# Performance work log

Measured on AMD Instinct MI355X. Metric: run time of the kernel, lower is better.

## Reference

```python
import jax, jax.numpy as jnp
import numpy as np


def setup_inputs() -> dict:
    key = jax.random.key(0)
    ks = jax.random.split(key, 7)
    B = 32768
    x = jax.random.normal(ks[0], (B, 1, 28, 28), dtype=jnp.float32)
    # learned params (AtomicLinear weight/bias per layer)
    w1 = jax.random.normal(ks[1], (128, 784), dtype=jnp.float32)
    b1 = jax.random.normal(ks[2], (128,), dtype=jnp.float32)
    w2 = jax.random.normal(ks[3], (256, 128), dtype=jnp.float32)
    b2 = jax.random.normal(ks[4], (256,), dtype=jnp.float32)
    w3 = jax.random.normal(ks[5], (10, 256), dtype=jnp.float32)
    b3 = jax.random.normal(ks[6], (10,), dtype=jnp.float32)
    return {"x": x, "w1": w1, "b1": b1, "w2": w2, "b2": b2, "w3": w3, "b3": b3}


def reference(x, w1, b1, w2, b2, w3, b3):
    # AtomicLinear: (x[:,None,:] * W) gathered by a random permutation over
    # in_features, then summed over that axis. Summation is permutation-
    # invariant, so this is exactly x @ W.T + b.
    B = x.shape[0]
    h = x.reshape(B, -1)                      # [B, 784]
    h = jax.nn.relu(h @ w1.T + b1)            # [B, 128]
    h = jax.nn.relu(h @ w2.T + b2)            # [B, 256]
    logits = h @ w3.T + b3                    # [B, 10]
    return jax.nn.log_softmax(logits, axis=1)
```

## Files before the change

### kernel.cpp

```cpp
#include <hip/hip_runtime.h>
#include <math.h>


#define TPB 512
#define BROWS 64

typedef __attribute__((ext_vector_type(8))) short bf16x8;
typedef __attribute__((ext_vector_type(4))) short bf16x4;
typedef __attribute__((ext_vector_type(4))) float f32x4;

static __device__ inline short f2bf(float f) {
    union { float f; unsigned u; } v; v.f = f;
    unsigned r = v.u + 0x7fffu + ((v.u >> 16) & 1u);
    return (short)(r >> 16);
}
static __device__ inline bf16x4 cvt4(float4 a) {
    bf16x4 r; r[0]=f2bf(a.x); r[1]=f2bf(a.y); r[2]=f2bf(a.z); r[3]=f2bf(a.w); return r;
}
static __device__ inline bf16x8 cvt8(float4 a, float4 b) {
    bf16x8 r;
    r[0]=f2bf(a.x); r[1]=f2bf(a.y); r[2]=f2bf(a.z); r[3]=f2bf(a.w);
    r[4]=f2bf(b.x); r[5]=f2bf(b.y); r[6]=f2bf(b.z); r[7]=f2bf(b.w);
    return r;
}
static __device__ inline float4 ld4g(const float* p, bool ok) {
    return ok ? *reinterpret_cast<const float4*>(p) : make_float4(0.f, 0.f, 0.f, 0.f);
}

__global__ __launch_bounds__(TPB, 4) void mnist_mfma_v2(
    const float* __restrict__ x,
    const float* __restrict__ w1,
    const float* __restrict__ b1,
    const float* __restrict__ w2,
    const float* __restrict__ b2,
    const float* __restrict__ w3,
    const float* __restrict__ b3,
    float* __restrict__ out)
{
    __shared__ __align__(16) char smem[40 * 1024];
    short* const s_w  = (short*)(smem);
    short* const s_x  = (short*)(smem + 16 * 1024);
    short* const s_h1 = (short*)(smem + 20 * 1024);
    short* const s_h2 = (short*)(smem);
    short* const s_w3 = (short*)(smem + 32 * 1024);

    const int t    = threadIdx.x;
    const int lane = t & 63;
    const int wv   = t >> 6;
    const int mi   = wv & 3;
    const int nh   = wv >> 2;
    const int l15  = lane & 15;
    const int l4   = lane >> 4;
    const int row0 = blockIdx.x * BROWS;

    const int xr = t >> 3, xs = t & 7;
    const int wn = t >> 2, ws = t & 3;

    f32x4 acc1[4];
    #pragma unroll
    for (int f = 0; f < 4; ++f) acc1[f] = (f32x4){0.f, 0.f, 0.f, 0.f};

    float4 xa = ld4g(&x[(size_t)(row0 + xr) * 784 + xs * 4], true);
    float4 wa = ld4g(&w1[(size_t)wn * 784 + ws * 8], true);
    float4 wb = ld4g(&w1[(size_t)wn * 784 + ws * 8 + 4], true);

    for (int kt = 0; kt < 25; ++kt) {
        __syncthreads();
        *reinterpret_cast<bf16x4*>(&s_x[xr * 32 + xs * 4]) = cvt4(xa);
        *reinterpret_cast<bf16x8*>(&s_w[wn * 32 + ws * 8]) = cvt8(wa, wb);
        if (kt < 24) {
            const int k0 = (kt + 1) * 32;
            xa = ld4g(&x[(size_t)(row0 + xr) * 784 + k0 + xs * 4], k0 + xs * 4 < 784);
            const bool okw = k0 + ws * 8 < 784;
            wa = ld4g(&w1[(size_t)wn * 784 + k0 + ws * 8], okw);
            wb = ld4g(&w1[(size_t)wn * 784 + k0 + ws * 8 + 4], okw);
        }
        __syncthreads();
        const bf16x8 a = *reinterpret_cast<const bf16x8*>(&s_x[(16 * mi + l15) * 32 + l4 * 8]);
        #pragma unroll
        for (int f = 0; f < 4; ++f) {
            const bf16x8 b = *reinterpret_cast<const bf16x8*>(
                &s_w[(nh * 64 + f * 16 + l15) * 32 + l4 * 8]);
            acc1[f] = __builtin_amdgcn_mfma_f32_16x16x32_bf16(a, b, acc1[f], 0, 0, 0);
        }
    }

    #pragma unroll
    for (int f = 0; f < 4; ++f) {
        const int c  = nh * 64 + f * 16 + l15;
        const float bc = b1[c];
        #pragma unroll
        for (int i = 0; i < 4; ++i) {
            const int r = 16 * mi + l4 * 4 + i;
            float h = acc1[f][i] + bc;
            h = h > 0.f ? h : 0.f;
            s_h1[r * 128 + ((((c >> 3) ^ (r & 7)) << 3) | (c & 7))] = f2bf(h);
        }
    }

    f32x4 acc2[8];
    #pragma unroll
    for (int f = 0; f < 8; ++f) acc2[f] = (f32x4){0.f, 0.f, 0.f, 0.f};

    float4 w2a0 = ld4g(&w2[(size_t)(t >> 2) * 128 + (t & 3) * 8], true);
    float4 w2b0 = ld4g(&w2[(size_t)(t >> 2) * 128 + (t & 3) * 8 + 4], true);
    float4 w2a1 = ld4g(&w2[(size_t)(128 + (t >> 2)) * 128 + (t & 3) * 8], true);
    float4 w2b1 = ld4g(&w2[(size_t)(128 + (t >> 2)) * 128 + (t & 3) * 8 + 4], true);
    float4 w3a, w3b;

    for (int kt = 0; kt < 4; ++kt) {
        __syncthreads();
        *reinterpret_cast<bf16x8*>(&s_w[(t >> 2) * 32 + (t & 3) * 8]) = cvt8(w2a0, w2b0);
        *reinterpret_cast<bf16x8*>(&s_w[(128 + (t >> 2)) * 32 + (t & 3) * 8]) = cvt8(w2a1, w2b1);
        if (kt < 3) {
            const int k0 = (kt + 1) * 32;
            w2a0 = ld4g(&w2[(size_t)(t >> 2) * 128 + k0 + (t & 3) * 8], true);
            w2b0 = ld4g(&w2[(size_t)(t >> 2) * 128 + k0 + (t & 3) * 8 + 4], true);
            w2a1 = ld4g(&w2[(size_t)(128 + (t >> 2)) * 128 + k0 + (t & 3) * 8], true);
            w2b1 = ld4g(&w2[(size_t)(128 + (t >> 2)) * 128 + k0 + (t & 3) * 8 + 4], true);
        } else {
            const int n3 = t >> 5, s3 = t & 31;
            const bool ok3 = n3 < 10;
            w3a = ld4g(&w3[(size_t)n3 * 256 + s3 * 8], ok3);
            w3b = ld4g(&w3[(size_t)n3 * 256 + s3 * 8 + 4], ok3);
        }
        __syncthreads();
        const bf16x8 a = *reinterpret_cast<const bf16x8*>(
            &s_h1[(16 * mi + l15) * 128 + (((kt * 4 + l4) ^ (l15 & 7)) << 3)]);
        #pragma unroll
        for (int f = 0; f < 8; ++f) {
            const bf16x8 b = *reinterpret_cast<const bf16x8*>(
                &s_w[(nh * 128 + f * 16 + l15) * 32 + l4 * 8]);
            acc2[f] = __builtin_amdgcn_mfma_f32_16x16x32_bf16(a, b, acc2[f], 0, 0, 0);
        }
    }

    __syncthreads();
    #pragma unroll
    for (int f = 0; f < 8; ++f) {
        const int c  = nh * 128 + f * 16 + l15;
        const float bc = b2[c];
        #pragma unroll
        for (int i = 0; i < 4; ++i) {
            const int r = 16 * mi + l4 * 4 + i;
            float h = acc2[f][i] + bc;
            h = h > 0.f ? h : 0.f;
            s_h2[r * 256 + ((((c >> 3) ^ (r & 7)) << 3) | (c & 7))] = f2bf(h);
        }
    }
    {
        const int n3 = t >> 5, s3 = t & 31;
        *reinterpret_cast<bf16x8*>(&s_w3[n3 * 256 + ((s3 ^ (n3 & 7)) << 3)]) = cvt8(w3a, w3b);
    }
    __syncthreads();

    if (nh == 0) {
        f32x4 acc3 = (f32x4){0.f, 0.f, 0.f, 0.f};
        #pragma unroll
        for (int kt = 0; kt < 8; ++kt) {
            const int slot = kt * 4 + l4;
            const bf16x8 a = *reinterpret_cast<const bf16x8*>(
                &s_h2[(16 * mi + l15) * 256 + ((slot ^ (l15 & 7)) << 3)]);
            const bf16x8 b = *reinterpret_cast<const bf16x8*>(
                &s_w3[l15 * 256 + ((slot ^ (l15 & 7)) << 3)]);
            acc3 = __builtin_amdgcn_mfma_f32_16x16x32_bf16(a, b, acc3, 0, 0, 0);
        }
        const float b3c = (l15 < 10) ? b3[l15] : 0.f;
        #pragma unroll
        for (int i = 0; i < 4; ++i) {
            const float v = acc3[i] + b3c;
            float m = (l15 < 10) ? v : -1e30f;
            #pragma unroll
            for (int off = 8; off; off >>= 1) m = fmaxf(m, __shfl_xor(m, off, 16));
            const float e = (l15 < 10) ? expf(v - m) : 0.f;
            float sum = e;
            #pragma unroll
            for (int off = 8; off; off >>= 1) sum += __shfl_xor(sum, off, 16);
            const float ls = m + logf(sum);
            if (l15 < 10) {
                const int r = row0 + 16 * mi + l4 * 4 + i;
                out[(size_t)r * 10 + l15] = v - ls;
            }
        }
    }
}

extern "C" void kernel_launch(void* const* d_in, const int* in_sizes, int n_in,
                              void* d_out, int out_size, void* d_ws, size_t ws_size,
                              hipStream_t stream) {
    const float* x  = (const float*)d_in[0];
    const float* w1 = (const float*)d_in[1];
    const float* b1 = (const float*)d_in[2];
    const float* w2 = (const float*)d_in[3];
    const float* b2 = (const float*)d_in[4];
    const float* w3 = (const float*)d_in[5];
    const float* b3 = (const float*)d_in[6];
    float* out = (float*)d_out;

    const int B = 32768;
    dim3 grid(B / BROWS), block(TPB);
    mnist_mfma_v2<<<grid, block, 0, stream>>>(x, w1, b1, w2, b2, w3, b3, out);
}
```

Baseline: 35.96 us.

## Pre-convert weights to bf16 and stream them to LDS with global_load_lds

A separate prep kernel converts w1, w2 and w3 to bf16 once per call, with padding, into a workspace buffer. The main kernel then copies weights straight into LDS with global_load_lds, double-buffering w1 in 128-wide K tiles. x is loaded from global directly into MFMA A fragments in registers instead of being staged through LDS, which cuts the K loop from 25 to 7 barrier-separated steps. The cost is an extra kernel launch, 64KB+16KB of LDS per block that may lower occupancy, and reliance on the async LDS load intrinsic.

```diff
diff --git a/kernel.cpp b/kernel.cpp
--- a/kernel.cpp
+++ b/kernel.cpp
@@ -5,17 +5,17 @@
 #define TPB 512
 #define BROWS 64
 
+#define W2OFF 114688
+#define W3OFF 147456
+#define WTOT  151552
+
 typedef __attribute__((ext_vector_type(8))) short bf16x8;
-typedef __attribute__((ext_vector_type(4))) short bf16x4;
 typedef __attribute__((ext_vector_type(4))) float f32x4;
 
 static __device__ inline short f2bf(float f) {
     union { float f; unsigned u; } v; v.f = f;
     unsigned r = v.u + 0x7fffu + ((v.u >> 16) & 1u);
     return (short)(r >> 16);
-}
-static __device__ inline bf16x4 cvt4(float4 a) {
-    bf16x4 r; r[0]=f2bf(a.x); r[1]=f2bf(a.y); r[2]=f2bf(a.z); r[3]=f2bf(a.w); return r;
 }
 static __device__ inline bf16x8 cvt8(float4 a, float4 b) {
     bf16x8 r;
@@ -24,25 +24,47 @@
     return r;
 }
 static __device__ inline float4 ld4g(const float* p, bool ok) {
-    return ok ? *reinterpret_cast<const float4*>(p) : make_float4(0.f, 0.f, 0.f, 0.f);
-}
-
-__global__ __launch_bounds__(TPB, 4) void mnist_mfma_v2(
+    return ok ? *reinterpret_cast<const float4*>(p) : make_float4(0.f,0.f,0.f,0.f);
+}
+static __device__ inline void gld16(const short* g, short* l) {
+    __builtin_amdgcn_global_load_lds(
+        (const __attribute__((address_space(1))) unsigned int*)g,
+        (__attribute__((address_space(3))) unsigned int*)l, 16, 0, 0);
+}
+
+__global__ void prep_weights(const float* __restrict__ w1,
+                             const float* __restrict__ w2,
+                             const float* __restrict__ w3,
+                             short* __restrict__ wb) {
+    const int idx = blockIdx.x * blockDim.x + threadIdx.x;
+    if (idx >= WTOT) return;
+    short v;
+    if (idx < W2OFF) {
+        const int r = idx / 896, k = idx - r * 896;
+        v = (k < 784) ? f2bf(w1[r * 784 + k]) : (short)0;
+    } else if (idx < W3OFF) {
+        v = f2bf(w2[idx - W2OFF]);
+    } else {
+        const int j = idx - W3OFF;
+        const int r = j >> 8, k = j & 255;
+        v = (r < 10) ? f2bf(w3[r * 256 + k]) : (short)0;
+    }
+    wb[idx] = v;
+}
+
+__global__ __launch_bounds__(TPB, 4) void mnist_v3(
     const float* __restrict__ x,
-    const float* __restrict__ w1,
-    const float* __restrict__ b1,
-    const float* __restrict__ w2,
-    const float* __restrict__ b2,
-    const float* __restrict__ w3,
-    const float* __restrict__ b3,
+    const float* __restrict__ b1v,
+    const float* __restrict__ b2v,
+    const float* __restrict__ b3v,
+    const short* __restrict__ wb,
     float* __restrict__ out)
 {
-    __shared__ __align__(16) char smem[40 * 1024];
-    short* const s_w  = (short*)(smem);
-    short* const s_x  = (short*)(smem + 16 * 1024);
-    short* const s_h1 = (short*)(smem + 20 * 1024);
-    short* const s_h2 = (short*)(smem);
-    short* const s_w3 = (short*)(smem + 32 * 1024);
+    __shared__ __align__(16) short s_w[2][16384];
+    __shared__ __align__(16) short s_h1[64 * 128];
+    short* const s_wf = &s_w[0][0];
+    short* const s_h2 = &s_w[0][0];
+    short* const s_w3 = &s_w[1][0];
 
     const int t    = threadIdx.x;
     const int lane = t & 63;
@@ -52,110 +74,122 @@
     const int l15  = lane & 15;
     const int l4   = lane >> 4;
     const int row0 = blockIdx.x * BROWS;
-
-    const int xr = t >> 3, xs = t & 7;
-    const int wn = t >> 2, ws = t & 3;
+    const int lr4  = lane >> 4;
+    const int ls16 = lane & 15;
 
     f32x4 acc1[4];
     #pragma unroll
-    for (int f = 0; f < 4; ++f) acc1[f] = (f32x4){0.f, 0.f, 0.f, 0.f};
-
-    float4 xa = ld4g(&x[(size_t)(row0 + xr) * 784 + xs * 4], true);
-    float4 wa = ld4g(&w1[(size_t)wn * 784 + ws * 8], true);
-    float4 wb = ld4g(&w1[(size_t)wn * 784 + ws * 8 + 4], true);
-
-    for (int kt = 0; kt < 25; ++kt) {
+    for (int f = 0; f < 4; ++f) acc1[f] = (f32x4){0.f,0.f,0.f,0.f};
+
+    #pragma unroll
+    for (int p = 0; p < 4; ++p) {
+        const int chunk = wv * 4 + p;
+        const int row   = chunk * 4 + lr4;
+        const int src   = row * 896 + ((ls16 ^ (row & 7)) << 3);
+        gld16(&wb[src], &s_w[0][chunk * 512]);
+    }
+    __syncthreads();
+
+    const float* xrow = &x[(size_t)(row0 + 16 * mi + l15) * 784];
+    for (int kt = 0; kt < 7; ++kt) {
+        const int cur = kt & 1;
+        const int k0  = kt * 128;
+        float4 xa[4], xb[4];
+        #pragma unroll
+        for (int kk = 0; kk < 4; ++kk) {
+            const int kg = k0 + kk * 32 + l4 * 8;
+            const bool ok = (kg + 8) <= 784;
+            xa[kk] = ld4g(xrow + kg, ok);
+            xb[kk] = ld4g(xrow + kg + 4, ok);
+        }
+        if (kt < 6) {
+            #pragma unroll
+            for (int p = 0; p < 4; ++p) {
+                const int chunk = wv * 4 + p;
+                const int row   = chunk * 4 + lr4;
+                const int src   = row * 896 + (kt + 1) * 128 + ((ls16 ^ (row & 7)) << 3);
+                gld16(&wb[src], &s_w[cur ^ 1][chunk * 512]);
+            }
+        }
+        bf16x8 a[4];
+        #pragma unroll
+        for (int kk = 0; kk < 4; ++kk) a[kk] = cvt8(xa[kk], xb[kk]);
+        #pragma unroll
+        for (int f = 0; f < 4; ++f) {
+            const int rB = nh * 64 + f * 16 + l15;
+            #pragma unroll
+            for (int kk = 0; kk < 4; ++kk) {
+                const bf16x8 b = *reinterpret_cast<const bf16x8*>(
+                    &s_w[cur][rB * 128 + (((kk * 4 + l4) ^ (l15 & 7)) << 3)]);
+                acc1[f] = __builtin_amdgcn_mfma_f32_16x16x32_bf16(a[kk], b, acc1[f], 0, 0, 0);
+            }
+        }
         __syncthreads();
-        *reinterpret_cast<bf16x4*>(&s_x[xr * 32 + xs * 4]) = cvt4(xa);
-        *reinterpret_cast<bf16x8*>(&s_w[wn * 32 + ws * 8]) = cvt8(wa, wb);
-        if (kt < 24) {
-            const int k0 = (kt + 1) * 32;
-            xa = ld4g(&x[(size_t)(row0 + xr) * 784 + k0 + xs * 4], k0 + xs * 4 < 784);
-            const bool okw = k0 + ws * 8 < 784;
-            wa = ld4g(&w1[(size_t)wn * 784 + k0 + ws * 8], okw);
-            wb = ld4g(&w1[(size_t)wn * 784 + k0 + ws * 8 + 4], okw);
-        }
-        __syncthreads();
-        const bf16x8 a = *reinterpret_cast<const bf16x8*>(&s_x[(16 * mi + l15) * 32 + l4 * 8]);
-        #pragma unroll
-        for (int f = 0; f < 4; ++f) {
-            const bf16x8 b = *reinterpret_cast<const bf16x8*>(
-                &s_w[(nh * 64 + f * 16 + l15) * 32 + l4 * 8]);
-            acc1[f] = __builtin_amdgcn_mfma_f32_16x16x32_bf16(a, b, acc1[f], 0, 0, 0);
-        }
-    }
-
+    }
+
+    #pragma unroll
+    for (int p = 0; p < 8; ++p) {
+        const int chunk = wv * 8 + p;
+        const int row   = chunk * 4 + lr4;
+        const int src   = W2OFF + row * 128 + ((ls16 ^ (row & 7)) << 3);
+        gld16(&wb[src], &s_wf[chunk * 512]);
+    }
     #pragma unroll
     for (int f = 0; f < 4; ++f) {
         const int c  = nh * 64 + f * 16 + l15;
-        const float bc = b1[c];
+        const float bc = b1v[c];
         #pragma unroll
         for (int i = 0; i < 4; ++i) {
             const int r = 16 * mi + l4 * 4 + i;
             float h = acc1[f][i] + bc;
             h = h > 0.f ? h : 0.f;
-            s_h1[r * 128 + ((((c >> 3) ^ (r & 7)) << 3) | (c & 7))] = f2bf(h);
-        }
-    }
+            s_h1[r * 128 + (((c >> 3) ^ (r & 7)) << 3) + (c & 7)] = f2bf(h);
+        }
+    }
+    __syncthreads();
 
     f32x4 acc2[8];
     #pragma unroll
-    for (int f = 0; f < 8; ++f) acc2[f] = (f32x4){0.f, 0.f, 0.f, 0.f};
-
-    float4 w2a0 = ld4g(&w2[(size_t)(t >> 2) * 128 + (t & 3) * 8], true);
-    float4 w2b0 = ld4g(&w2[(size_t)(t >> 2) * 128 + (t & 3) * 8 + 4], true);
-    float4 w2a1 = ld4g(&w2[(size_t)(128 + (t >> 2)) * 128 + (t & 3) * 8], true);
-    float4 w2b1 = ld4g(&w2[(size_t)(128 + (t >> 2)) * 128 + (t & 3) * 8 + 4], true);
-    float4 w3a, w3b;
-
-    for (int kt = 0; kt < 4; ++kt) {
-        __syncthreads();
-        *reinterpret_cast<bf16x8*>(&s_w[(t >> 2) * 32 + (t & 3) * 8]) = cvt8(w2a0, w2b0);
-        *reinterpret_cast<bf16x8*>(&s_w[(128 + (t >> 2)) * 32 + (t & 3) * 8]) = cvt8(w2a1, w2b1);
-        if (kt < 3) {
-            const int k0 = (kt + 1) * 32;
-            w2a0 = ld4g(&w2[(size_t)(t >> 2) * 128 + k0 + (t & 3) * 8], true);
-            w2b0 = ld4g(&w2[(size_t)(t >> 2) * 128 + k0 + (t & 3) * 8 + 4], true);
-            w2a1 = ld4g(&w2[(size_t)(128 + (t >> 2)) * 128 + k0 + (t & 3) * 8], true);
-            w2b1 = ld4g(&w2[(size_t)(128 + (t >> 2)) * 128 + k0 + (t & 3) * 8 + 4], true);
-        } else {
-            const int n3 = t >> 5, s3 = t & 31;
-            const bool ok3 = n3 < 10;
-            w3a = ld4g(&w3[(size_t)n3 * 256 + s3 * 8], ok3);
-            w3b = ld4g(&w3[(size_t)n3 * 256 + s3 * 8 + 4], ok3);
-        }
-        __syncthreads();
-        const bf16x8 a = *reinterpret_cast<const bf16x8*>(
-            &s_h1[(16 * mi + l15) * 128 + (((kt * 4 + l4) ^ (l15 & 7)) << 3)]);
-        #pragma unroll
-        for (int f = 0; f < 8; ++f) {
+    for (int f = 0; f < 8; ++f) acc2[f] = (f32x4){0.f,0.f,0.f,0.f};
+    bf16x8 a2[4];
+    #pragma unroll
+    for (int kk = 0; kk < 4; ++kk)
+        a2[kk] = *reinterpret_cast<const bf16x8*>(
+            &s_h1[(16 * mi + l15) * 128 + (((kk * 4 + l4) ^ (l15 & 7)) << 3)]);
+    #pragma unroll
+    for (int f = 0; f < 8; ++f) {
+        const int rB = nh * 128 + f * 16 + l15;
+        #pragma unroll
+        for (int kk = 0; kk < 4; ++kk) {
             const bf16x8 b = *reinterpret_cast<const bf16x8*>(
-                &s_w[(nh * 128 + f * 16 + l15) * 32 + l4 * 8]);
-            acc2[f] = __builtin_amdgcn_mfma_f32_16x16x32_bf16(a, b, acc2[f], 0, 0, 0);
-        }
-    }
-
-    __syncthreads();
+                &s_wf[rB * 128 + (((kk * 4 + l4) ^ (l15 & 7)) << 3)]);
+            acc2[f] = __builtin_amdgcn_mfma_f32_16x16x32_bf16(a2[kk], b, acc2[f], 0, 0, 0);
+        }
+    }
+    __syncthreads();
+
+    {
+        const int row = wv * 2 + (lane >> 5);
+        const int sp  = lane & 31;
+        const int src = W3OFF + row * 256 + ((sp ^ (row & 7)) << 3);
+        gld16(&wb[src], &s_w3[wv * 512]);
+    }
     #pragma unroll
     for (int f = 0; f < 8; ++f) {
         const int c  = nh * 128 + f * 16 + l15;
-        const float bc = b2[c];
+        const float bc = b2v[c];
         #pragma unroll
         for (int i = 0; i < 4; ++i) {
             const int r = 16 * mi + l4 * 4 + i;
             float h = acc2[f][i] + bc;
             h = h > 0.f ? h : 0.f;
-            s_h2[r * 256 + ((((c >> 3) ^ (r & 7)) << 3) | (c & 7))] = f2bf(h);
-        }
-    }
-    {
-        const int n3 = t >> 5, s3 = t & 31;
-        *reinterpret_cast<bf16x8*>(&s_w3[n3 * 256 + ((s3 ^ (n3 & 7)) << 3)]) = cvt8(w3a, w3b);
+            s_h2[r * 256 + (((c >> 3) ^ (r & 7)) << 3) + (c & 7)] = f2bf(h);
+        }
     }
     __syncthreads();
 
     if (nh == 0) {
-        f32x4 acc3 = (f32x4){0.f, 0.f, 0.f, 0.f};
+        f32x4 acc3 = (f32x4){0.f,0.f,0.f,0.f};
         #pragma unroll
         for (int kt = 0; kt < 8; ++kt) {
             const int slot = kt * 4 + l4;
@@ -165,7 +199,7 @@
                 &s_w3[l15 * 256 + ((slot ^ (l15 & 7)) << 3)]);
             acc3 = __builtin_amdgcn_mfma_f32_16x16x32_bf16(a, b, acc3, 0, 0, 0);
         }
-        const float b3c = (l15 < 10) ? b3[l15] : 0.f;
+        const float b3c = (l15 < 10) ? b3v[l15] : 0.f;
         #pragma unroll
         for (int i = 0; i < 4; ++i) {
             const float v = acc3[i] + b3c;
@@ -196,8 +230,11 @@
     const float* w3 = (const float*)d_in[5];
     const float* b3 = (const float*)d_in[6];
     float* out = (float*)d_out;
+    short* wb  = (short*)d_ws;
+
+    prep_weights<<<(WTOT + TPB - 1) / TPB, TPB, 0, stream>>>(w1, w2, w3, wb);
 
     const int B = 32768;
     dim3 grid(B / BROWS), block(TPB);
-    mnist_mfma_v2<<<grid, block, 0, stream>>>(x, w1, b1, w2, b2, w3, b3, out);
-}
+    mnist_v3<<<grid, block, 0, stream>>>(x, b1, b2, b3, wb, out);
+}
```

Result: slower. 42.09 us (+17.1%).
